# Kernel tuning notes

Measured on AMD Instinct MI355X. Metric: run time of the kernel, lower is better.

The kernel has to match this reference:

```python
import jax, jax.numpy as jnp
import numpy as np

S, B, I, H = 2048, 64, 128, 128
E = float(np.e)


def setup_inputs() -> dict:
    key = jax.random.key(0)
    ks = jax.random.split(key, 16)
    s = 1.0 / np.sqrt(H)
    inp = {
        "x": jax.random.normal(ks[0], (S, B, I), jnp.float32),
        "h0": jnp.zeros((2, B, H), jnp.float32),
        "c0": jnp.zeros((2, B, H), jnp.float32),
        # elapsed times, strictly positive
        "delta_ts": jax.random.uniform(ks[1], (B, S), jnp.float32, 0.1, 10.0),
    }
    names = ["W_ih", "W_hh", "b_ih", "b_hh", "W_d", "b_d"]
    shapes = [(4 * H, I), (4 * H, H), (4 * H,), (4 * H,), (H, H), (H,)]
    idx = 2
    for d in ["f", "r"]:
        for n, sh in zip(names, shapes):
            inp[f"{n}_{d}"] = jax.random.uniform(ks[idx], sh, jnp.float32, -s, s)
            idx += 1
    return inp


def _run_dir(x, dt, h, c, W_ih, W_hh, b_ih, b_hh, W_d, b_d):
    """Scan a TLSTM cell over time. x: [S,B,I], dt: [S,B]."""
    def step(carry, inp):
        h, c = carry
        xt, dtt = inp
        # time-aware memory decomposition (Baytas et al.)
        c_s = jnp.tanh(c @ W_d.T + b_d)               # short-term memory
        c_adj = c - c_s + c_s / jnp.log(E + dtt[:, None])  # discounted by elapsed time
        gates = xt @ W_ih.T + b_ih + h @ W_hh.T + b_hh
        i_g, f_g, g_g, o_g = jnp.split(gates, 4, axis=-1)
        c_n = jax.nn.sigmoid(f_g) * c_adj + jax.nn.sigmoid(i_g) * jnp.tanh(g_g)
        h_n = jax.nn.sigmoid(o_g) * jnp.tanh(c_n)
        return (h_n, c_n), h_n

    (h, c), ys = jax.lax.scan(step, (h, c), (x, dt))
    return ys, h, c


def reference(x, h0, c0, delta_ts,
              W_ih_f, W_hh_f, b_ih_f, b_hh_f, W_d_f, b_d_f,
              W_ih_r, W_hh_r, b_ih_r, b_hh_r, W_d_r, b_d_r):
    dt = delta_ts.T  # [S, B]
    out_f, _, _ = _run_dir(x, dt, h0[0], c0[0],
                           W_ih_f, W_hh_f, b_ih_f, b_hh_f, W_d_f, b_d_f)
    out_r, _, _ = _run_dir(x[::-1], dt[::-1], h0[1], c0[1],
                           W_ih_r, W_hh_r, b_ih_r, b_hh_r, W_d_r, b_d_r)
    return jnp.concatenate([out_f, out_r[::-1]], axis=-1)  # [S, B, 2H]
```

## Files before the change

kernel.cpp:

```cpp
#include <hip/hip_runtime.h>
#include <hip/hip_bf16.h>

#define SEQ  2048
#define BAT  64
#define HID  128
#define LDSP 136

#define XB_OFF  (1u << 20)
#define IL_OFF  (35u << 20)

typedef __bf16 bf16x8 __attribute__((ext_vector_type(8)));
typedef float  f32x4  __attribute__((ext_vector_type(4)));

#define MFMA(a,b,c) __builtin_amdgcn_mfma_f32_16x16x32_bf16((a),(b),(c),0,0,0)

__device__ __forceinline__ float sig_f(float x) {
    return __fdividef(1.0f, 1.0f + __expf(-x));
}
__device__ __forceinline__ float tanh_f(float x) {
    return 1.0f - __fdividef(2.0f, 1.0f + __expf(2.0f * x));
}
__device__ __forceinline__ bf16x8 cvt8(const float* p) {
    bf16x8 r;
    #pragma unroll
    for (int i = 0; i < 8; ++i) r[i] = (__bf16)p[i];
    return r;
}

__global__ void cvt_x_kernel(const float* __restrict__ x, __bf16* __restrict__ xb) {
    const int i = (blockIdx.x * 256 + threadIdx.x) * 4;
    const float4 v = *reinterpret_cast<const float4*>(x + i);
    __bf16 o[4];
    o[0] = (__bf16)v.x; o[1] = (__bf16)v.y; o[2] = (__bf16)v.z; o[3] = (__bf16)v.w;
    *reinterpret_cast<uint2*>(xb + i) = *reinterpret_cast<const uint2*>(o);
}

__global__ void prep_ilog_kernel(const float* __restrict__ dts, float* __restrict__ il) {
    const int idx = blockIdx.x * 256 + threadIdx.x;
    const int b = idx >> 11, t = idx & 2047;
    const float l = __logf(2.718281828459045f + dts[idx]);
    il[t * BAT + b] = __fdividef(1.0f, l) - 1.0f;
}

__global__ __launch_bounds__(512, 2) void tlstm_main(
    const __bf16* __restrict__ xb,   const float* __restrict__ ilg,
    const float* __restrict__ h0,    const float* __restrict__ c0,
    const float* __restrict__ Wih_f, const float* __restrict__ Whh_f,
    const float* __restrict__ bih_f, const float* __restrict__ bhh_f,
    const float* __restrict__ Wd_f,  const float* __restrict__ bd_f,
    const float* __restrict__ Wih_r, const float* __restrict__ Whh_r,
    const float* __restrict__ bih_r, const float* __restrict__ bhh_r,
    const float* __restrict__ Wd_r,  const float* __restrict__ bd_r,
    float* __restrict__ out)
{
    const int d    = blockIdx.x >> 4;
    const int b0   = (blockIdx.x & 15) * 4;
    const int tid  = threadIdx.x;
    const int w    = tid >> 6;
    const int lane = tid & 63;
    const int nl   = lane & 15;
    const int q    = lane >> 4;
    const int j    = w * 16 + nl;

    const float* Wih = d ? Wih_r : Wih_f;
    const float* Whh = d ? Whh_r : Whh_f;
    const float* bih = d ? bih_r : bih_f;
    const float* bhh = d ? bhh_r : bhh_f;
    const float* Wd  = d ? Wd_r  : Wd_f;
    const float* bd  = d ? bd_r  : bd_f;

    __shared__ __align__(16) __bf16 hc_a[2][16][LDSP];

    bf16x8 whh_fr[4][4], wih_fr[4][4], wd_fr[4];
    #pragma unroll
    for (int g = 0; g < 4; ++g) {
        const int row = g * 128 + j;
        #pragma unroll
        for (int kt = 0; kt < 4; ++kt) {
            const int off = row * HID + kt * 32 + q * 8;
            wih_fr[g][kt] = cvt8(Wih + off);
            whh_fr[g][kt] = cvt8(Whh + off);
        }
    }
    #pragma unroll
    for (int kt = 0; kt < 4; ++kt)
        wd_fr[kt] = cvt8(Wd + j * HID + kt * 32 + q * 8);

    f32x4 bgv[4];
    #pragma unroll
    for (int g = 0; g < 4; ++g) {
        const float b = bih[g * 128 + j] + bhh[g * 128 + j];
        bgv[g] = f32x4{b, b, b, b};
    }
    const float bias_d = bd[j];
    const f32x4 bdv = f32x4{bias_d, bias_d, bias_d, bias_d};

    for (int e = tid; e < 4 * HID; e += 512) {
        const int ci = e >> 7, k = e & 127;
        hc_a[0][ci * 4][k]     = (__bf16)h0[(d * BAT + b0 + ci) * HID + k];
        hc_a[0][ci * 4 + 2][k] = (__bf16)c0[(d * BAT + b0 + ci) * HID + k];
    }
    float c_st = c0[(d * BAT + b0 + q) * HID + j];
    __syncthreads();

    const int t0      = d ? (SEQ - 1) : 0;
    const int tstep   = d ? -1 : 1;
    const int xstride = tstep * BAT * HID;
    const int istride = tstep * BAT;
    const int ostride = tstep * BAT * 256;

    const __bf16* xp0 = xb + (size_t)((t0 + tstep * (nl & 3)) * BAT + b0 + (nl >> 2)) * HID + q * 8;
    const float*  ip0 = ilg + (size_t)t0 * BAT + b0 + q;
    float*        op  = out + (size_t)(t0 * BAT + b0 + q) * 256 + d * 128 + j;

    bf16x8 X0[4], X1[4];
    f32x4  xaccA[4], xaccB[4];
    float  ilA[4], ilB[4];

    {
        bf16x8 t[4];
        #pragma unroll
        for (int kt = 0; kt < 4; ++kt)
            t[kt] = *reinterpret_cast<const bf16x8*>(xp0 + kt * 32);
        xaccA[0] = MFMA(t[0], wih_fr[0][0], bgv[0]);
        xaccA[1] = MFMA(t[0], wih_fr[1][0], bgv[1]);
        xaccA[2] = MFMA(t[0], wih_fr[2][0], bgv[2]);
        xaccA[3] = MFMA(t[0], wih_fr[3][0], bgv[3]);
        #pragma unroll
        for (int kt = 1; kt < 4; ++kt) {
            xaccA[0] = MFMA(t[kt], wih_fr[0][kt], xaccA[0]);
            xaccA[1] = MFMA(t[kt], wih_fr[1][kt], xaccA[1]);
            xaccA[2] = MFMA(t[kt], wih_fr[2][kt], xaccA[2]);
            xaccA[3] = MFMA(t[kt], wih_fr[3][kt], xaccA[3]);
        }
    }
    #pragma unroll
    for (int kt = 0; kt < 4; ++kt) {
        X1[kt] = *reinterpret_cast<const bf16x8*>(xp0 + 4 * xstride + kt * 32);
        X0[kt] = *reinterpret_cast<const bf16x8*>(xp0 + 8 * xstride + kt * 32);
    }
    #pragma unroll
    for (int dtv = 0; dtv < 4; ++dtv) {
        ilA[dtv] = ip0[dtv * istride];
        ilB[dtv] = ip0[(4 + dtv) * istride];
    }
    const __bf16* xpl = xp0 + 8 * xstride;
    const float*  ipl = ip0 + 8 * istride;

    auto chunk = [&](f32x4 (&xu)[4], f32x4 (&xnb)[4],
                     bf16x8 (&xfS)[4], bf16x8 (&xfL)[4],
                     float (&ilCur)[4]) __attribute__((always_inline)) {
        #pragma unroll
        for (int dt = 0; dt < 4; ++dt) {
            const int p  = dt & 1;
            const int pn = p ^ 1;
            const int hr = dt;
            const int cr = (dt + 2) & 3;

            const float il_use = ilCur[dt];

            bf16x8 hcfr[4];
            #pragma unroll
            for (int kt = 0; kt < 4; ++kt)
                hcfr[kt] = *reinterpret_cast<const bf16x8*>(&hc_a[p][nl][kt * 32 + q * 8]);

            xfL[dt]    = *reinterpret_cast<const bf16x8*>(xpl + dt * 32);
            ilCur[dt]  = ipl[dt * istride];

            f32x4 cA = MFMA(hcfr[0], wd_fr[0],     bdv);
            f32x4 g0 = MFMA(hcfr[0], whh_fr[0][0], xu[0]);
            f32x4 g1 = MFMA(hcfr[0], whh_fr[1][0], xu[1]);
            f32x4 g2 = MFMA(hcfr[0], whh_fr[2][0], xu[2]);
            f32x4 g3 = MFMA(hcfr[0], whh_fr[3][0], xu[3]);
            #pragma unroll
            for (int kt = 1; kt < 4; ++kt) {
                cA = MFMA(hcfr[kt], wd_fr[kt],      cA);
                g0 = MFMA(hcfr[kt], whh_fr[0][kt],  g0);
                g1 = MFMA(hcfr[kt], whh_fr[1][kt],  g1);
                g2 = MFMA(hcfr[kt], whh_fr[2][kt],  g2);
                g3 = MFMA(hcfr[kt], whh_fr[3][kt],  g3);
            }

            {
                f32x4 xs = MFMA(xfS[0], wih_fr[dt][0], bgv[dt]);
                xs       = MFMA(xfS[1], wih_fr[dt][1], xs);
                xs       = MFMA(xfS[2], wih_fr[dt][2], xs);
                xnb[dt]  = MFMA(xfS[3], wih_fr[dt][3], xs);
            }

            {
                const float cs   = tanh_f(cA[cr]);
                const float cadj = fmaf(cs, il_use, c_st);
                const float gf   = sig_f(g1[hr]);
                const float gi   = sig_f(g0[hr]);
                const float gg   = tanh_f(g2[hr]);
                const float cn   = gf * cadj + gi * gg;
                hc_a[pn][q * 4 + ((dt + 3) & 3)][j] = (__bf16)cn;
                const float go   = sig_f(g3[hr]);
                const float hn   = go * tanh_f(cn);
                c_st = cn;
                hc_a[pn][q * 4 + ((dt + 1) & 3)][j] = (__bf16)hn;
                *op = hn;
            }
            op += ostride;

            asm volatile("s_waitcnt lgkmcnt(0)\n\ts_barrier" ::: "memory");
        }
        xpl += 4 * xstride;
        ipl += 4 * istride;
    };

    for (int tc = 0; tc < SEQ / 4; tc += 2) {
        chunk(xaccA, xaccB, X1, X0, ilA);
        chunk(xaccB, xaccA, X0, X1, ilB);
    }
}

extern "C" void kernel_launch(void* const* d_in, const int* in_sizes, int n_in,
                              void* d_out, int out_size, void* d_ws, size_t ws_size,
                              hipStream_t stream) {
    const float* x     = (const float*)d_in[0];
    const float* h0    = (const float*)d_in[1];
    const float* c0    = (const float*)d_in[2];
    const float* dts   = (const float*)d_in[3];
    const float* Wih_f = (const float*)d_in[4];
    const float* Whh_f = (const float*)d_in[5];
    const float* bih_f = (const float*)d_in[6];
    const float* bhh_f = (const float*)d_in[7];
    const float* Wd_f  = (const float*)d_in[8];
    const float* bd_f  = (const float*)d_in[9];
    const float* Wih_r = (const float*)d_in[10];
    const float* Whh_r = (const float*)d_in[11];
    const float* bih_r = (const float*)d_in[12];
    const float* bhh_r = (const float*)d_in[13];
    const float* Wd_r  = (const float*)d_in[14];
    const float* bd_r  = (const float*)d_in[15];
    float* out = (float*)d_out;

    __bf16* xbuf = (__bf16*)((char*)d_ws + XB_OFF);
    float*  il   = (float*)((char*)d_ws + IL_OFF);

    cvt_x_kernel<<<16384, 256, 0, stream>>>(x, xbuf);
    prep_ilog_kernel<<<512, 256, 0, stream>>>(dts, il);

    tlstm_main<<<32, 512, 0, stream>>>(xbuf, il, h0, c0,
                                       Wih_f, Whh_f, bih_f, bhh_f, Wd_f, bd_f,
                                       Wih_r, Whh_r, bih_r, bhh_r, Wd_r, bd_r,
                                       out);
}
```

Measured before the change: 2.216 ms.

## Precompute input gate projections in a parallel GEMM and pack two batch groups per recurrent block

A new xg_kernel computes x@W_ih^T plus biases for all timesteps and both directions in one highly parallel MFMA pass, storing packed float4 gate preactivations in workspace (about 512MB). The recurrent kernel then only does the h/c MFMAs, and each block now handles 8 batch rows (two 16-row MFMA tiles) on 16 blocks instead of 32. This removes the input projection from the serial critical path and gives each barrier step more independent MFMA work. In exchange it adds a large fp32 intermediate round-trip through HBM, needs enough workspace (otherwise a fallback path runs), and may lengthen each serial step.

```diff
diff --git a/kernel.cpp b/kernel.cpp
--- a/kernel.cpp
+++ b/kernel.cpp
@@ -8,6 +8,8 @@
 
 #define XB_OFF  (1u << 20)
 #define IL_OFF  (35u << 20)
+#define XG_OFF  ((size_t)36 << 20)
+#define WS_NEED ((size_t)(36 + 512 + 1) << 20)
 
 typedef __bf16 bf16x8 __attribute__((ext_vector_type(8)));
 typedef float  f32x4  __attribute__((ext_vector_type(4)));
@@ -42,7 +44,225 @@
     il[t * BAT + b] = __fdividef(1.0f, l) - 1.0f;
 }
 
-__global__ __launch_bounds__(512, 2) void tlstm_main(
+__global__ __launch_bounds__(512, 2) void xg_kernel(
+    const __bf16* __restrict__ xb,
+    const float* __restrict__ Wih_f, const float* __restrict__ bih_f, const float* __restrict__ bhh_f,
+    const float* __restrict__ Wih_r, const float* __restrict__ bih_r, const float* __restrict__ bhh_r,
+    float4* __restrict__ xg)
+{
+    const int tid  = threadIdx.x;
+    const int w    = tid >> 6;
+    const int lane = tid & 63;
+    const int nl   = lane & 15;
+    const int q    = lane >> 4;
+    const int j    = w * 16 + nl;
+
+    bf16x8 wf[2][4][4];
+    f32x4  bg[2][4];
+    #pragma unroll
+    for (int g = 0; g < 4; ++g) {
+        const int row = g * 128 + j;
+        #pragma unroll
+        for (int kt = 0; kt < 4; ++kt) {
+            const int off = row * HID + kt * 32 + q * 8;
+            wf[0][g][kt] = cvt8(Wih_f + off);
+            wf[1][g][kt] = cvt8(Wih_r + off);
+        }
+        const float bf = bih_f[row] + bhh_f[row];
+        const float br = bih_r[row] + bhh_r[row];
+        bg[0][g] = f32x4{bf, bf, bf, bf};
+        bg[1][g] = f32x4{br, br, br, br};
+    }
+
+    for (int it = 0; it < 8; ++it) {
+        const int Mt = it * 1024 + blockIdx.x;
+        bf16x8 afr[4];
+        #pragma unroll
+        for (int kt = 0; kt < 4; ++kt)
+            afr[kt] = *reinterpret_cast<const bf16x8*>(xb + (size_t)(Mt * 16 + nl) * HID + kt * 32 + q * 8);
+
+        #pragma unroll
+        for (int dd = 0; dd < 2; ++dd) {
+            f32x4 a0 = MFMA(afr[0], wf[dd][0][0], bg[dd][0]);
+            f32x4 a1 = MFMA(afr[0], wf[dd][1][0], bg[dd][1]);
+            f32x4 a2 = MFMA(afr[0], wf[dd][2][0], bg[dd][2]);
+            f32x4 a3 = MFMA(afr[0], wf[dd][3][0], bg[dd][3]);
+            #pragma unroll
+            for (int kt = 1; kt < 4; ++kt) {
+                a0 = MFMA(afr[kt], wf[dd][0][kt], a0);
+                a1 = MFMA(afr[kt], wf[dd][1][kt], a1);
+                a2 = MFMA(afr[kt], wf[dd][2][kt], a2);
+                a3 = MFMA(afr[kt], wf[dd][3][kt], a3);
+            }
+            #pragma unroll
+            for (int r = 0; r < 4; ++r) {
+                const int row = Mt * 16 + 4 * q + r;
+                xg[((size_t)dd * SEQ * BAT + row) * HID + j] = float4{a0[r], a1[r], a2[r], a3[r]};
+            }
+        }
+    }
+}
+
+__global__ __launch_bounds__(512, 2) void tlstm_dual(
+    const float4* __restrict__ xg,  const float* __restrict__ ilg,
+    const float* __restrict__ h0,   const float* __restrict__ c0,
+    const float* __restrict__ Whh_f, const float* __restrict__ Wd_f, const float* __restrict__ bd_f,
+    const float* __restrict__ Whh_r, const float* __restrict__ Wd_r, const float* __restrict__ bd_r,
+    float* __restrict__ out)
+{
+    const int d    = blockIdx.x >> 3;
+    const int b0   = (blockIdx.x & 7) * 8;
+    const int tid  = threadIdx.x;
+    const int w    = tid >> 6;
+    const int lane = tid & 63;
+    const int nl   = lane & 15;
+    const int q    = lane >> 4;
+    const int j    = w * 16 + nl;
+
+    const float* Whh = d ? Whh_r : Whh_f;
+    const float* Wd  = d ? Wd_r  : Wd_f;
+    const float* bd  = d ? bd_r  : bd_f;
+
+    __shared__ __align__(16) __bf16 hc[2][2][16][LDSP];
+
+    bf16x8 whh_fr[4][4], wd_fr[4];
+    #pragma unroll
+    for (int g = 0; g < 4; ++g) {
+        const int row = g * 128 + j;
+        #pragma unroll
+        for (int kt = 0; kt < 4; ++kt)
+            whh_fr[g][kt] = cvt8(Whh + row * HID + kt * 32 + q * 8);
+    }
+    #pragma unroll
+    for (int kt = 0; kt < 4; ++kt)
+        wd_fr[kt] = cvt8(Wd + j * HID + kt * 32 + q * 8);
+
+    const float bias_d = bd[j];
+    const f32x4 bdv = f32x4{bias_d, bias_d, bias_d, bias_d};
+    const f32x4 zc  = f32x4{0.0f, 0.0f, 0.0f, 0.0f};
+
+    for (int e = tid; e < 8 * HID; e += 512) {
+        const int ci = e >> 7, k = e & 127;
+        const int grp = ci >> 2, cl = ci & 3;
+        hc[grp][0][cl * 4][k]     = (__bf16)h0[(d * BAT + b0 + ci) * HID + k];
+        hc[grp][0][cl * 4 + 1][k] = (__bf16)c0[(d * BAT + b0 + ci) * HID + k];
+    }
+    float c_st0 = c0[(d * BAT + b0 + q) * HID + j];
+    float c_st1 = c0[(d * BAT + b0 + 4 + q) * HID + j];
+    __syncthreads();
+
+    const int t0    = d ? (SEQ - 1) : 0;
+    const int tstep = d ? -1 : 1;
+    const long xgstep = (long)tstep * BAT * HID;
+    const int  istride = tstep * BAT;
+    const int  ostride = tstep * BAT * 256;
+
+    const float4* xg0 = xg + ((size_t)d * SEQ * BAT + (size_t)t0 * BAT + b0 + q) * HID + j;
+    const float4* xg1 = xg0 + (size_t)4 * HID;
+    const float*  ip0 = ilg + (size_t)t0 * BAT + b0 + q;
+    const float*  ip1 = ip0 + 4;
+    float* op0 = out + (size_t)(t0 * BAT + b0 + q) * 256 + d * 128 + j;
+    float* op1 = op0 + 4 * 256;
+
+    float4 xgb0[4], xgb1[4];
+    float  ilb0[4], ilb1[4];
+    #pragma unroll
+    for (int s = 0; s < 4; ++s) {
+        xgb0[s] = xg0[(long)s * xgstep];
+        xgb1[s] = xg1[(long)s * xgstep];
+        ilb0[s] = ip0[s * istride];
+        ilb1[s] = ip1[s * istride];
+    }
+    const float4* xgl0 = xg0 + 4 * xgstep;
+    const float4* xgl1 = xg1 + 4 * xgstep;
+    const float*  ill0 = ip0 + 4 * istride;
+    const float*  ill1 = ip1 + 4 * istride;
+
+    for (int ts = 0; ts < SEQ; ts += 4) {
+        #pragma unroll
+        for (int dt = 0; dt < 4; ++dt) {
+            const int p  = dt & 1;
+            const int pn = p ^ 1;
+
+            bf16x8 hcfr0[4], hcfr1[4];
+            #pragma unroll
+            for (int kt = 0; kt < 4; ++kt)
+                hcfr0[kt] = *reinterpret_cast<const bf16x8*>(&hc[0][p][nl][kt * 32 + q * 8]);
+            #pragma unroll
+            for (int kt = 0; kt < 4; ++kt)
+                hcfr1[kt] = *reinterpret_cast<const bf16x8*>(&hc[1][p][nl][kt * 32 + q * 8]);
+
+            const float4 xv0 = xgb0[dt]; const float il0 = ilb0[dt];
+            const float4 xv1 = xgb1[dt]; const float il1 = ilb1[dt];
+            xgb0[dt] = *xgl0; xgl0 += xgstep;
+            xgb1[dt] = *xgl1; xgl1 += xgstep;
+            ilb0[dt] = *ill0; ill0 += istride;
+            ilb1[dt] = *ill1; ill1 += istride;
+
+            f32x4 cA0 = MFMA(hcfr0[0], wd_fr[0],     bdv);
+            f32x4 a00 = MFMA(hcfr0[0], whh_fr[0][0], zc);
+            f32x4 a01 = MFMA(hcfr0[0], whh_fr[1][0], zc);
+            f32x4 a02 = MFMA(hcfr0[0], whh_fr[2][0], zc);
+            f32x4 a03 = MFMA(hcfr0[0], whh_fr[3][0], zc);
+            #pragma unroll
+            for (int kt = 1; kt < 4; ++kt) {
+                cA0 = MFMA(hcfr0[kt], wd_fr[kt],     cA0);
+                a00 = MFMA(hcfr0[kt], whh_fr[0][kt], a00);
+                a01 = MFMA(hcfr0[kt], whh_fr[1][kt], a01);
+                a02 = MFMA(hcfr0[kt], whh_fr[2][kt], a02);
+                a03 = MFMA(hcfr0[kt], whh_fr[3][kt], a03);
+            }
+            f32x4 cA1 = MFMA(hcfr1[0], wd_fr[0],     bdv);
+            f32x4 a10 = MFMA(hcfr1[0], whh_fr[0][0], zc);
+            f32x4 a11 = MFMA(hcfr1[0], whh_fr[1][0], zc);
+            f32x4 a12 = MFMA(hcfr1[0], whh_fr[2][0], zc);
+            f32x4 a13 = MFMA(hcfr1[0], whh_fr[3][0], zc);
+            #pragma unroll
+            for (int kt = 1; kt < 4; ++kt) {
+                cA1 = MFMA(hcfr1[kt], wd_fr[kt],     cA1);
+                a10 = MFMA(hcfr1[kt], whh_fr[0][kt], a10);
+                a11 = MFMA(hcfr1[kt], whh_fr[1][kt], a11);
+                a12 = MFMA(hcfr1[kt], whh_fr[2][kt], a12);
+                a13 = MFMA(hcfr1[kt], whh_fr[3][kt], a13);
+            }
+
+            {
+                const float cs   = tanh_f(cA0[1]);
+                const float cadj = fmaf(cs, il0, c_st0);
+                const float gi   = sig_f(a00[0] + xv0.x);
+                const float gf   = sig_f(a01[0] + xv0.y);
+                const float gg   = tanh_f(a02[0] + xv0.z);
+                const float cn   = gf * cadj + gi * gg;
+                hc[0][pn][q * 4 + 1][j] = (__bf16)cn;
+                const float go   = sig_f(a03[0] + xv0.w);
+                const float hn   = go * tanh_f(cn);
+                c_st0 = cn;
+                hc[0][pn][q * 4][j] = (__bf16)hn;
+                *op0 = hn;
+            }
+            op0 += ostride;
+            {
+                const float cs   = tanh_f(cA1[1]);
+                const float cadj = fmaf(cs, il1, c_st1);
+                const float gi   = sig_f(a10[0] + xv1.x);
+                const float gf   = sig_f(a11[0] + xv1.y);
+                const float gg   = tanh_f(a12[0] + xv1.z);
+                const float cn   = gf * cadj + gi * gg;
+                hc[1][pn][q * 4 + 1][j] = (__bf16)cn;
+                const float go   = sig_f(a13[0] + xv1.w);
+                const float hn   = go * tanh_f(cn);
+                c_st1 = cn;
+                hc[1][pn][q * 4][j] = (__bf16)hn;
+                *op1 = hn;
+            }
+            op1 += ostride;
+
+            asm volatile("s_waitcnt lgkmcnt(0)\n\ts_barrier" ::: "memory");
+        }
+    }
+}
+
+__global__ __launch_bounds__(512, 2) void tlstm_fb(
     const __bf16* __restrict__ xb,   const float* __restrict__ ilg,
     const float* __restrict__ h0,    const float* __restrict__ c0,
     const float* __restrict__ Wih_f, const float* __restrict__ Whh_f,
@@ -113,7 +333,7 @@
     const float*  ip0 = ilg + (size_t)t0 * BAT + b0 + q;
     float*        op  = out + (size_t)(t0 * BAT + b0 + q) * 256 + d * 128 + j;
 
-    bf16x8 X0[4], X1[4];
+    bf16x8 xfrA[4], xfrB[4];
     f32x4  xaccA[4], xaccB[4];
     float  ilA[4], ilB[4];
 
@@ -136,8 +356,8 @@
     }
     #pragma unroll
     for (int kt = 0; kt < 4; ++kt) {
-        X1[kt] = *reinterpret_cast<const bf16x8*>(xp0 + 4 * xstride + kt * 32);
-        X0[kt] = *reinterpret_cast<const bf16x8*>(xp0 + 8 * xstride + kt * 32);
+        xfrA[kt] = *reinterpret_cast<const bf16x8*>(xp0 + 4 * xstride + kt * 32);
+        xfrB[kt] = *reinterpret_cast<const bf16x8*>(xp0 + 8 * xstride + kt * 32);
     }
     #pragma unroll
     for (int dtv = 0; dtv < 4; ++dtv) {
@@ -150,6 +370,19 @@
     auto chunk = [&](f32x4 (&xu)[4], f32x4 (&xnb)[4],
                      bf16x8 (&xfS)[4], bf16x8 (&xfL)[4],
                      float (&ilCur)[4]) __attribute__((always_inline)) {
+        f32x4 n0 = MFMA(xfS[0], wih_fr[0][0], bgv[0]);
+        f32x4 n1 = MFMA(xfS[0], wih_fr[1][0], bgv[1]);
+        f32x4 n2 = MFMA(xfS[0], wih_fr[2][0], bgv[2]);
+        f32x4 n3 = MFMA(xfS[0], wih_fr[3][0], bgv[3]);
+        #pragma unroll
+        for (int kt = 1; kt < 4; ++kt) {
+            n0 = MFMA(xfS[kt], wih_fr[0][kt], n0);
+            n1 = MFMA(xfS[kt], wih_fr[1][kt], n1);
+            n2 = MFMA(xfS[kt], wih_fr[2][kt], n2);
+            n3 = MFMA(xfS[kt], wih_fr[3][kt], n3);
+        }
+        xnb[0] = n0; xnb[1] = n1; xnb[2] = n2; xnb[3] = n3;
+
         #pragma unroll
         for (int dt = 0; dt < 4; ++dt) {
             const int p  = dt & 1;
@@ -164,8 +397,8 @@
             for (int kt = 0; kt < 4; ++kt)
                 hcfr[kt] = *reinterpret_cast<const bf16x8*>(&hc_a[p][nl][kt * 32 + q * 8]);
 
-            xfL[dt]    = *reinterpret_cast<const bf16x8*>(xpl + dt * 32);
-            ilCur[dt]  = ipl[dt * istride];
+            xfL[dt]   = *reinterpret_cast<const bf16x8*>(xpl + dt * 32);
+            ilCur[dt] = ipl[dt * istride];
 
             f32x4 cA = MFMA(hcfr[0], wd_fr[0],     bdv);
             f32x4 g0 = MFMA(hcfr[0], whh_fr[0][0], xu[0]);
@@ -179,13 +412,6 @@
                 g1 = MFMA(hcfr[kt], whh_fr[1][kt],  g1);
                 g2 = MFMA(hcfr[kt], whh_fr[2][kt],  g2);
                 g3 = MFMA(hcfr[kt], whh_fr[3][kt],  g3);
-            }
-
-            {
-                f32x4 xs = MFMA(xfS[0], wih_fr[dt][0], bgv[dt]);
-                xs       = MFMA(xfS[1], wih_fr[dt][1], xs);
-                xs       = MFMA(xfS[2], wih_fr[dt][2], xs);
-                xnb[dt]  = MFMA(xfS[3], wih_fr[dt][3], xs);
             }
 
             {
@@ -211,8 +437,8 @@
     };
 
     for (int tc = 0; tc < SEQ / 4; tc += 2) {
-        chunk(xaccA, xaccB, X1, X0, ilA);
-        chunk(xaccB, xaccA, X0, X1, ilB);
+        chunk(xaccA, xaccB, xfrA, xfrB, ilA);
+        chunk(xaccB, xaccA, xfrB, xfrA, ilB);
     }
 }
 
@@ -243,8 +469,17 @@
     cvt_x_kernel<<<16384, 256, 0, stream>>>(x, xbuf);
     prep_ilog_kernel<<<512, 256, 0, stream>>>(dts, il);
 
-    tlstm_main<<<32, 512, 0, stream>>>(xbuf, il, h0, c0,
-                                       Wih_f, Whh_f, bih_f, bhh_f, Wd_f, bd_f,
-                                       Wih_r, Whh_r, bih_r, bhh_r, Wd_r, bd_r,
-                                       out);
-}
+    if (ws_size >= WS_NEED) {
+        float4* xg = (float4*)((char*)d_ws + XG_OFF);
+        xg_kernel<<<1024, 512, 0, stream>>>(xbuf, Wih_f, bih_f, bhh_f,
+                                            Wih_r, bih_r, bhh_r, xg);
+        tlstm_dual<<<16, 512, 0, stream>>>(xg, il, h0, c0,
+                                           Whh_f, Wd_f, bd_f,
+                                           Whh_r, Wd_r, bd_r, out);
+    } else {
+        tlstm_fb<<<32, 512, 0, stream>>>(xbuf, il, h0, c0,
+                                         Wih_f, Whh_f, bih_f, bhh_f, Wd_f, bd_f,
+                                         Wih_r, Whh_r, bih_r, bhh_r, Wd_r, bd_r,
+                                         out);
+    }
+}
```

After: 2.619 ms. 18.2% more time.
